# Kernel tuning notes

Measured on AMD Instinct MI355X. Metric: run time of the kernel, lower is better.

Reference implementation:

```python
import jax, jax.numpy as jnp
import numpy as np

CH = 64
CF = CH // 8  # f/g projection channels


def setup_inputs() -> dict:
    key = jax.random.key(0)
    k1, k2, k3, k4, k5 = jax.random.split(key, 5)
    x = jax.random.normal(k1, (8, 64, 64, CH), dtype=jnp.float32)
    kernel_f = 0.02 * jax.random.normal(k2, (1, 1, CH, CF), dtype=jnp.float32)
    kernel_g = 0.02 * jax.random.normal(k3, (1, 1, CH, CF), dtype=jnp.float32)
    kernel_h = 0.02 * jax.random.normal(k4, (1, 1, CH, CH), dtype=jnp.float32)
    gamma = 0.02 * jax.random.normal(k5, (1,), dtype=jnp.float32)
    return {"x": x, "kernel_f": kernel_f, "kernel_g": kernel_g,
            "kernel_h": kernel_h, "gamma": gamma}


def reference(x, kernel_f, kernel_g, kernel_h, gamma):
    B, H, W, C = x.shape
    N = H * W
    xf = x.reshape(B, N, C)  # flatten spatial; 1x1 conv == matmul over channels
    f = jnp.einsum('bnc,cd->bnd', xf, kernel_f[0, 0])  # [B,N,CF]
    g = jnp.einsum('bnc,cd->bnd', xf, kernel_g[0, 0])  # [B,N,CF]
    h = jnp.einsum('bnc,cd->bnd', xf, kernel_h[0, 0])  # [B,N,C]
    s = jnp.einsum('bnd,bmd->bnm', g, f)  # g @ f^T, [B,N,N]
    beta = jax.nn.softmax(s, axis=-1)
    o = jnp.einsum('bnm,bmc->bnc', beta, h)  # [B,N,C]
    out = gamma * o.reshape(B, H, W, C) + x
    return out
```

## Files before the change

### kernel.cpp

```cpp
#include <hip/hip_runtime.h>
#include <hip/hip_bf16.h>

typedef __attribute__((ext_vector_type(4)))  float f32x4;
typedef __attribute__((ext_vector_type(16))) float f32x16;
typedef __attribute__((ext_vector_type(8)))  short bf16x8;

#define LOG2E 1.44269504088896340736f

#if __has_builtin(__builtin_amdgcn_exp2f)
static __device__ __forceinline__ float exp2_native(float x) {
  return __builtin_amdgcn_exp2f(x);
}
#else
extern "C" __device__ float __ocml_native_exp2_f32(float);
static __device__ __forceinline__ float exp2_native(float x) {
  return __ocml_native_exp2_f32(x);
}
#endif

static __device__ __forceinline__ unsigned int pack_trunc_f(float a, float b) {
  return __builtin_amdgcn_perm(__float_as_uint(b), __float_as_uint(a), 0x07060302);
}

typedef const __attribute__((address_space(1))) unsigned int gu32;
typedef __attribute__((address_space(3))) unsigned int lu32;
static __device__ __forceinline__ void gload_lds16(const void* g, void* l) {
  __builtin_amdgcn_global_load_lds((gu32*)g, (lu32*)l, 16, 0, 0);
}

__global__ __launch_bounds__(256) void proj_kernel(
    const float* __restrict__ x, const float* __restrict__ kf,
    const float* __restrict__ kg, const float* __restrict__ kh,
    unsigned short* __restrict__ f_b, unsigned short* __restrict__ g_b,
    unsigned short* __restrict__ h_p)
{
  __shared__ unsigned short Kt[80*72];
  const int t = threadIdx.x, blk = blockIdx.x;

  #pragma unroll
  for (int r = 0; r < 20; ++r) {
    int idx = r*256 + t;
    int o = idx >> 6, c = idx & 63;
    float v = (o < 8) ? kf[c*8 + o]
            : (o < 16) ? kg[c*8 + (o-8)] * LOG2E
            : kh[c*64 + (o-16)];
    Kt[o*72 + c] = (unsigned short)(__float_as_uint(v) >> 16);
  }
  __syncthreads();

  const int w = t >> 6, lane = t & 63, l15 = lane & 15, quad = lane >> 4;
  const int Rbase = blk*64 + w*16;
  const int R = Rbase + l15;

  bf16x8 af[2];
  #pragma unroll
  for (int kk = 0; kk < 2; ++kk) {
    const float* xp = x + (long)R*64 + kk*32 + quad*8;
    float4 v0 = *(const float4*)xp;
    float4 v1 = *(const float4*)(xp + 4);
    union { unsigned int u[4]; bf16x8 v; } p;
    p.u[0] = pack_trunc_f(v0.x, v0.y);
    p.u[1] = pack_trunc_f(v0.z, v0.w);
    p.u[2] = pack_trunc_f(v1.x, v1.y);
    p.u[3] = pack_trunc_f(v1.z, v1.w);
    af[kk] = p.v;
  }

  f32x4 acc[5];
  #pragma unroll
  for (int nt = 0; nt < 5; ++nt) { f32x4 z = {}; acc[nt] = z; }

  #pragma unroll
  for (int nt = 0; nt < 5; ++nt)
    #pragma unroll
    for (int kk = 0; kk < 2; ++kk) {
      bf16x8 bfv = *(const bf16x8*)&Kt[(nt*16 + l15)*72 + kk*32 + quad*8];
      acc[nt] = __builtin_amdgcn_mfma_f32_16x16x32_bf16(af[kk], bfv, acc[nt], 0, 0, 0);
    }

  const int bt = Rbase >> 12;
  const int kt = (Rbase >> 7) & 31;
  const int base = ((blk & 1) << 6) + (w << 4);
  const int pi = base + ((quad & 1) << 3) + (((quad >> 1) & 1) << 2);

  #pragma unroll
  for (int rr = 0; rr < 4; ++rr) {
    const int nq = (Rbase + quad*4 + rr) & 4095;
    unsigned short v = (unsigned short)(__float_as_uint(acc[0][rr]) >> 16);
    if (l15 < 8) f_b[((long)bt*4096 + nq)*8 + l15] = v;
    else         g_b[((long)bt*4096 + nq)*8 + (l15 - 8)] = v;
  }
  #pragma unroll
  for (int nt = 1; nt < 5; ++nt) {
    const int c = (nt - 1)*16 + l15;
    uint2 v;
    v.x = pack_trunc_f(acc[nt][0], acc[nt][1]);
    v.y = pack_trunc_f(acc[nt][2], acc[nt][3]);
    *(uint2*)(h_p + ((long)(bt*32 + kt)*64 + c)*136 + pi) = v;
  }
}

__global__ __launch_bounds__(128, 2) void attn_kernel(
    const unsigned short* __restrict__ f_b, const unsigned short* __restrict__ g_b,
    const unsigned short* __restrict__ h_p, unsigned short* __restrict__ po,
    float* __restrict__ pl)
{
  __shared__ unsigned short bufs[2][9728];

  const int t = threadIdx.x;
  const int w = t >> 6, lane = t & 63, l31 = lane & 31, a = lane >> 5;
  const int qb = blockIdx.x, b = blockIdx.y, sp = blockIdx.z;
  const int q0w = qb*128 + w*64;

  bf16x8 gf[2];
  #pragma unroll
  for (int qg = 0; qg < 2; ++qg) {
    bf16x8 gv = *(const bf16x8*)(g_b + ((long)b*4096 + q0w + qg*32 + l31)*8);
    bf16x8 z = {};
    gf[qg] = (a == 0) ? gv : z;
  }

  f32x16 oacc[2][2];
  { f32x16 z = {}; oacc[0][0] = z; oacc[0][1] = z; oacc[1][0] = z; oacc[1][1] = z; }
  float l_run[2] = {0.f, 0.f};

  const char* hp_b = (const char*)h_p + (long)b*32*17408;
  const char* fb_b = (const char*)f_b + (long)b*4096*16;

  auto stage = [&](int bi, int kt) {
    const char* hsrc = hp_b + (long)kt*17408;
    const char* fsrc = fb_b + (long)kt*2048;
    char* dst = (char*)&bufs[bi][0];
    #pragma unroll
    for (int i = 0; i < 8; ++i)
      gload_lds16(hsrc + i*2048 + w*1024 + lane*16, dst + i*2048 + w*1024);
    if (w == 0) {
      gload_lds16(hsrc + 16384 + lane*16, dst + 16384);
    } else {
      gload_lds16(fsrc + lane*16,        dst + 17408);
      gload_lds16(fsrc + 1024 + lane*16, dst + 17408 + 1024);
    }
  };

  stage(0, sp*8);

  for (int ktl = 0; ktl < 8; ++ktl) {
    __syncthreads();
    if (ktl < 7) stage((ktl + 1) & 1, sp*8 + ktl + 1);

    const unsigned short* hts = &bufs[ktl & 1][0];
    const unsigned short* fts = &bufs[ktl & 1][8704];

    #pragma unroll
    for (int mt = 0; mt < 4; ++mt) {
      bf16x8 afv = *(const bf16x8*)&fts[(mt*32 + l31)*8];
      f32x16 zz = {};
      f32x16 sc0 = __builtin_amdgcn_mfma_f32_32x32x16_bf16(afv, gf[0], zz, 0, 0, 0);
      f32x16 sc1 = __builtin_amdgcn_mfma_f32_32x32x16_bf16(afv, gf[1], zz, 0, 0, 0);

      float e0[16], e1[16];
      #pragma unroll
      for (int r = 0; r < 16; ++r) {
        e0[r] = exp2_native(sc0[r]);
        e1[r] = exp2_native(sc1[r]);
        l_run[0] += e0[r];
        l_run[1] += e1[r];
      }

      #pragma unroll
      for (int half = 0; half < 2; ++half) {
        const int s = mt*2 + half;
        bf16x8 bh0 = *(const bf16x8*)&hts[(l31)*136      + s*16 + a*8];
        bf16x8 bh1 = *(const bf16x8*)&hts[(32 + l31)*136 + s*16 + a*8];
        union { unsigned int u[4]; bf16x8 v; } ap0, ap1;
        #pragma unroll
        for (int j = 0; j < 4; ++j) {
          ap0.u[j] = pack_trunc_f(e0[half*8 + 2*j], e0[half*8 + 2*j + 1]);
          ap1.u[j] = pack_trunc_f(e1[half*8 + 2*j], e1[half*8 + 2*j + 1]);
        }
        oacc[0][0] = __builtin_amdgcn_mfma_f32_32x32x16_bf16(ap0.v, bh0, oacc[0][0], 0, 0, 0);
        oacc[0][1] = __builtin_amdgcn_mfma_f32_32x32x16_bf16(ap0.v, bh1, oacc[0][1], 0, 0, 0);
        oacc[1][0] = __builtin_amdgcn_mfma_f32_32x32x16_bf16(ap1.v, bh0, oacc[1][0], 0, 0, 0);
        oacc[1][1] = __builtin_amdgcn_mfma_f32_32x32x16_bf16(ap1.v, bh1, oacc[1][1], 0, 0, 0);
      }
    }
  }

  const long sb = (long)sp*8 + b;
  #pragma unroll
  for (int qg = 0; qg < 2; ++qg) {
    float l = l_run[qg] + __shfl_xor(l_run[qg], 32);
    if (lane < 32) pl[(sb << 12) + q0w + qg*32 + l31] = l;
    unsigned short* pob = po + ((sb << 12) + q0w + qg*32)*64;
    #pragma unroll
    for (int nt = 0; nt < 2; ++nt)
      #pragma unroll
      for (int r = 0; r < 16; ++r) {
        const int q = (r & 3) + 8*(r >> 2) + 4*a;
        pob[(long)q*64 + nt*32 + l31] =
            (unsigned short)(__float_as_uint(oacc[qg][nt][r]) >> 16);
      }
  }
}

__global__ __launch_bounds__(256) void combine_kernel(
    const float* __restrict__ x, const unsigned short* __restrict__ po,
    const float* __restrict__ pl, const float* __restrict__ gamma_p,
    float* __restrict__ out)
{
  const long tid = (long)blockIdx.x*256 + threadIdx.x;
  const long bn = tid >> 3;
  const int c0 = (int)(tid & 7)*8;

  float l = 0.f;
  float o[8];
  #pragma unroll
  for (int i = 0; i < 8; ++i) o[i] = 0.f;
  #pragma unroll
  for (int s = 0; s < 4; ++s) {
    l += pl[(long)s*32768 + bn];
    uint4 v = *(const uint4*)(po + ((long)s*32768 + bn)*64 + c0);
    const unsigned short* pv = (const unsigned short*)&v;
    #pragma unroll
    for (int i = 0; i < 8; ++i)
      o[i] += __uint_as_float((unsigned int)pv[i] << 16);
  }
  const float scale = gamma_p[0] / l;
  const float* xp = x + bn*64 + c0;
  float4 x0 = *(const float4*)xp;
  float4 x1 = *(const float4*)(xp + 4);
  float4 r0, r1;
  r0.x = fmaf(scale, o[0], x0.x);
  r0.y = fmaf(scale, o[1], x0.y);
  r0.z = fmaf(scale, o[2], x0.z);
  r0.w = fmaf(scale, o[3], x0.w);
  r1.x = fmaf(scale, o[4], x1.x);
  r1.y = fmaf(scale, o[5], x1.y);
  r1.z = fmaf(scale, o[6], x1.z);
  r1.w = fmaf(scale, o[7], x1.w);
  float* op = out + bn*64 + c0;
  *(float4*)op = r0;
  *(float4*)(op + 4) = r1;
}

extern "C" void kernel_launch(void* const* d_in, const int* in_sizes, int n_in,
                              void* d_out, int out_size, void* d_ws, size_t ws_size,
                              hipStream_t stream) {
  const float* x  = (const float*)d_in[0];
  const float* kf = (const float*)d_in[1];
  const float* kg = (const float*)d_in[2];
  const float* kh = (const float*)d_in[3];
  const float* gamma = (const float*)d_in[4];
  float* out = (float*)d_out;

  char* ws = (char*)d_ws;
  unsigned short* h_p = (unsigned short*)ws;
  unsigned short* f_b = (unsigned short*)(ws + 4456448);
  unsigned short* g_b = (unsigned short*)(ws + 4980736);
  unsigned short* po  = (unsigned short*)(ws + 5505024);
  float*          pl  = (float*)(ws + 22282240);

  proj_kernel<<<512, 256, 0, stream>>>(x, kf, kg, kh, f_b, g_b, h_p);
  attn_kernel<<<dim3(32, 8, 4), 128, 0, stream>>>(f_b, g_b, h_p, po, pl);
  combine_kernel<<<1024, 256, 0, stream>>>(x, po, pl, gamma, out);
}
```

Baseline: 102.8 us.

## Split attention work across four waves with 32 queries each to raise occupancy

```diff
diff --git a/kernel.cpp b/kernel.cpp
--- a/kernel.cpp
+++ b/kernel.cpp
@@ -100,7 +100,7 @@
   }
 }
 
-__global__ __launch_bounds__(128, 2) void attn_kernel(
+__global__ __launch_bounds__(256, 4) void attn_kernel(
     const unsigned short* __restrict__ f_b, const unsigned short* __restrict__ g_b,
     const unsigned short* __restrict__ h_p, unsigned short* __restrict__ po,
     float* __restrict__ pl)
@@ -110,19 +110,18 @@
   const int t = threadIdx.x;
   const int w = t >> 6, lane = t & 63, l31 = lane & 31, a = lane >> 5;
   const int qb = blockIdx.x, b = blockIdx.y, sp = blockIdx.z;
-  const int q0w = qb*128 + w*64;
-
-  bf16x8 gf[2];
-  #pragma unroll
-  for (int qg = 0; qg < 2; ++qg) {
-    bf16x8 gv = *(const bf16x8*)(g_b + ((long)b*4096 + q0w + qg*32 + l31)*8);
+  const int q0w = qb*128 + w*32;
+
+  bf16x8 gfv;
+  {
+    bf16x8 gv = *(const bf16x8*)(g_b + ((long)b*4096 + q0w + l31)*8);
     bf16x8 z = {};
-    gf[qg] = (a == 0) ? gv : z;
-  }
-
-  f32x16 oacc[2][2];
-  { f32x16 z = {}; oacc[0][0] = z; oacc[0][1] = z; oacc[1][0] = z; oacc[1][1] = z; }
-  float l_run[2] = {0.f, 0.f};
+    gfv = (a == 0) ? gv : z;
+  }
+
+  f32x16 oacc[2];
+  { f32x16 z = {}; oacc[0] = z; oacc[1] = z; }
+  float l_run = 0.f;
 
   const char* hp_b = (const char*)h_p + (long)b*32*17408;
   const char* fb_b = (const char*)f_b + (long)b*4096*16;
@@ -132,13 +131,12 @@
     const char* fsrc = fb_b + (long)kt*2048;
     char* dst = (char*)&bufs[bi][0];
     #pragma unroll
-    for (int i = 0; i < 8; ++i)
-      gload_lds16(hsrc + i*2048 + w*1024 + lane*16, dst + i*2048 + w*1024);
-    if (w == 0) {
-      gload_lds16(hsrc + 16384 + lane*16, dst + 16384);
-    } else {
-      gload_lds16(fsrc + lane*16,        dst + 17408);
-      gload_lds16(fsrc + 1024 + lane*16, dst + 17408 + 1024);
+    for (int i = 0; i < 5; ++i) {
+      const int off = i*4096 + w*1024;
+      if (off < 19456) {
+        const char* src = (off < 17408) ? (hsrc + off) : (fsrc + (off - 17408));
+        gload_lds16(src + lane*16, dst + off);
+      }
     }
   };
 
@@ -155,52 +153,40 @@
     for (int mt = 0; mt < 4; ++mt) {
       bf16x8 afv = *(const bf16x8*)&fts[(mt*32 + l31)*8];
       f32x16 zz = {};
-      f32x16 sc0 = __builtin_amdgcn_mfma_f32_32x32x16_bf16(afv, gf[0], zz, 0, 0, 0);
-      f32x16 sc1 = __builtin_amdgcn_mfma_f32_32x32x16_bf16(afv, gf[1], zz, 0, 0, 0);
-
-      float e0[16], e1[16];
-      #pragma unroll
-      for (int r = 0; r < 16; ++r) {
-        e0[r] = exp2_native(sc0[r]);
-        e1[r] = exp2_native(sc1[r]);
-        l_run[0] += e0[r];
-        l_run[1] += e1[r];
-      }
+      f32x16 sc = __builtin_amdgcn_mfma_f32_32x32x16_bf16(afv, gfv, zz, 0, 0, 0);
 
       #pragma unroll
       for (int half = 0; half < 2; ++half) {
         const int s = mt*2 + half;
         bf16x8 bh0 = *(const bf16x8*)&hts[(l31)*136      + s*16 + a*8];
         bf16x8 bh1 = *(const bf16x8*)&hts[(32 + l31)*136 + s*16 + a*8];
-        union { unsigned int u[4]; bf16x8 v; } ap0, ap1;
+        union { unsigned int u[4]; bf16x8 v; } ap;
         #pragma unroll
         for (int j = 0; j < 4; ++j) {
-          ap0.u[j] = pack_trunc_f(e0[half*8 + 2*j], e0[half*8 + 2*j + 1]);
-          ap1.u[j] = pack_trunc_f(e1[half*8 + 2*j], e1[half*8 + 2*j + 1]);
+          float ea = exp2_native(sc[half*8 + 2*j]);
+          float eb = exp2_native(sc[half*8 + 2*j + 1]);
+          l_run += ea;
+          l_run += eb;
+          ap.u[j] = pack_trunc_f(ea, eb);
         }
-        oacc[0][0] = __builtin_amdgcn_mfma_f32_32x32x16_bf16(ap0.v, bh0, oacc[0][0], 0, 0, 0);
-        oacc[0][1] = __builtin_amdgcn_mfma_f32_32x32x16_bf16(ap0.v, bh1, oacc[0][1], 0, 0, 0);
-        oacc[1][0] = __builtin_amdgcn_mfma_f32_32x32x16_bf16(ap1.v, bh0, oacc[1][0], 0, 0, 0);
-        oacc[1][1] = __builtin_amdgcn_mfma_f32_32x32x16_bf16(ap1.v, bh1, oacc[1][1], 0, 0, 0);
+        oacc[0] = __builtin_amdgcn_mfma_f32_32x32x16_bf16(ap.v, bh0, oacc[0], 0, 0, 0);
+        oacc[1] = __builtin_amdgcn_mfma_f32_32x32x16_bf16(ap.v, bh1, oacc[1], 0, 0, 0);
       }
     }
   }
 
   const long sb = (long)sp*8 + b;
-  #pragma unroll
-  for (int qg = 0; qg < 2; ++qg) {
-    float l = l_run[qg] + __shfl_xor(l_run[qg], 32);
-    if (lane < 32) pl[(sb << 12) + q0w + qg*32 + l31] = l;
-    unsigned short* pob = po + ((sb << 12) + q0w + qg*32)*64;
-    #pragma unroll
-    for (int nt = 0; nt < 2; ++nt)
-      #pragma unroll
-      for (int r = 0; r < 16; ++r) {
-        const int q = (r & 3) + 8*(r >> 2) + 4*a;
-        pob[(long)q*64 + nt*32 + l31] =
-            (unsigned short)(__float_as_uint(oacc[qg][nt][r]) >> 16);
-      }
-  }
+  float l = l_run + __shfl_xor(l_run, 32);
+  if (lane < 32) pl[(sb << 12) + q0w + l31] = l;
+  unsigned short* pob = po + ((sb << 12) + q0w)*64;
+  #pragma unroll
+  for (int nt = 0; nt < 2; ++nt)
+    #pragma unroll
+    for (int r = 0; r < 16; ++r) {
+      const int q = (r & 3) + 8*(r >> 2) + 4*a;
+      pob[(long)q*64 + nt*32 + l31] =
+          (unsigned short)(__float_as_uint(oacc[nt][r]) >> 16);
+    }
 }
 
 __global__ __launch_bounds__(256) void combine_kernel(
@@ -261,6 +247,6 @@
   float*          pl  = (float*)(ws + 22282240);
 
   proj_kernel<<<512, 256, 0, stream>>>(x, kf, kg, kh, f_b, g_b, h_p);
-  attn_kernel<<<dim3(32, 8, 4), 128, 0, stream>>>(f_b, g_b, h_p, po, pl);
+  attn_kernel<<<dim3(32, 8, 4), 256, 0, stream>>>(f_b, g_b, h_p, po, pl);
   combine_kernel<<<1024, 256, 0, stream>>>(x, po, pl, gamma, out);
 }
```

New measurement: 104.3 us. No clear change (+1.5%).
